# Kernel tuning notes

Hardware: AMD Instinct MI355X
Metric: run time of the kernel (lower is better)

The kernel has to match this reference:

```python
import jax, jax.numpy as jnp
import numpy as np

BLOCK_SIZE = 32
TAU = 0.1
E2M1_VALUES = np.array([0.0, 0.5, 1.0, 1.5, 2.0, 3.0, 4.0, 6.0], dtype=np.float32)
E2M1_BOUNDS = np.array([0.25, 0.75, 1.25, 1.75, 2.5, 3.5, 5.0], dtype=np.float32)


def setup_inputs() -> dict:
    key = jax.random.key(0)
    x = jax.random.normal(key, (2048, 4096), dtype=jnp.float32)
    return {
        "x": x,
        "delta_raw": jnp.zeros((), dtype=jnp.float32),
        "bounds_base": jnp.asarray(E2M1_BOUNDS),
        "values_table": jnp.asarray(E2M1_VALUES),
    }


def reference(x, delta_raw, bounds_base, values_table):
    orig_shape = x.shape
    bs = BLOCK_SIZE
    xb = x.reshape(-1, bs)  # [n_blocks, bs]
    # per-block e8m0 power-of-two scale from amax
    amax = jnp.max(jnp.abs(xb), axis=-1, keepdims=True)
    descale = amax / 6.0
    e8m0_scale = jnp.ceil(jnp.maximum(jnp.log2(descale), -127.0))
    scale_factor = jnp.exp2(e8m0_scale)
    x_scaled = (xb / scale_factor).reshape(orig_shape)
    # perturbed decision bounds
    shifted_bounds = bounds_base + 0.5 * jnp.tanh(delta_raw)  # [7]
    x_abs = jnp.abs(x_scaled)
    # hard ordinal bucketize: count bounds exceeded -> code in [0,7]
    ord_hard = jnp.sum(x_abs[..., None] > shifted_bounds, axis=-1)  # int32
    sign_bit = (x_scaled < 0).astype(jnp.uint8)
    codes = (sign_bit << 3) | ord_hard.astype(jnp.uint8)
    # soft ordinal weights via sigmoid at each boundary
    p = jax.nn.sigmoid((x_abs[..., None] - shifted_bounds) / TAU)  # [..., 7]
    w0 = 1.0 - p[..., 0]
    mids = p[..., :-1] - p[..., 1:]
    w_last = p[..., -1]
    weights = jnp.concatenate([w0[..., None], mids, w_last[..., None]], axis=-1)  # [..., 8]
    weights = jnp.clip(weights, 0.0)
    weights = weights / (jnp.sum(weights, axis=-1, keepdims=True) + 1e-8)
    abs_soft = jnp.sum(weights * values_table, axis=-1)
    abs_hard = values_table[ord_hard]
    # straight-through: hard value forward, soft gradient
    abs_mix = abs_soft + jax.lax.stop_gradient(abs_hard - abs_soft)
    y_scaled = jnp.where(x_scaled >= 0, abs_mix, -abs_mix)
    y = (y_scaled.reshape(-1, bs) * scale_factor).reshape(orig_shape)
    scales = (e8m0_scale + 127.0).astype(jnp.uint8)[:, 0].reshape(
        *orig_shape[:-1], orig_shape[-1] // bs
    )
    return (y, codes, scales, shifted_bounds, weights)
```

## Files before the change

kernel.cpp:

```cpp
#include <hip/hip_runtime.h>

#define BLK 256

__global__ __launch_bounds__(BLK) void fp4_kernel(
    const float* __restrict__ x,
    const float* __restrict__ delta_raw,
    const float* __restrict__ bounds_base,
    const float* __restrict__ values_table,
    float* __restrict__ out, long long N)
{
    const int tid = threadIdx.x;
    const long long gid = (long long)blockIdx.x * BLK + tid;

    __shared__ float s_vals[8];
    __shared__ float s_w[8 * 264];

    if (tid < 8) s_vals[tid] = values_table[tid];

    const float delta = delta_raw[0];
    const float ht = 0.5f * tanhf(delta);
    float sb[7];
#pragma unroll
    for (int j = 0; j < 7; ++j) sb[j] = bounds_base[j] + ht;

    __syncthreads();

    const float xi = x[gid];

    float a = fabsf(xi);
#pragma unroll
    for (int off = 16; off >= 1; off >>= 1)
        a = fmaxf(a, __shfl_xor(a, off, 32));

    const float descale = a / 6.0f;
    const float e = ceilf(fmaxf(log2f(descale), -127.0f));
    const float scale = exp2f(e);
    const float xs = xi / scale;
    const float xa = fabsf(xs);

    int ord = 0;
    float p[7];
#pragma unroll
    for (int j = 0; j < 7; ++j) {
        if (xa > sb[j]) ord++;
        p[j] = 1.0f / (1.0f + expf(-((xa - sb[j]) / 0.1f)));
    }

    float w[8];
    w[0] = 1.0f - p[0];
#pragma unroll
    for (int j = 1; j < 7; ++j) w[j] = p[j - 1] - p[j];
    w[7] = p[6];

    float sum = 0.0f;
#pragma unroll
    for (int k = 0; k < 8; ++k) { w[k] = fmaxf(w[k], 0.0f); sum += w[k]; }
    const float inv = 1.0f / (sum + 1e-8f);

    float abs_soft = 0.0f;
#pragma unroll
    for (int k = 0; k < 8; ++k) { w[k] *= inv; abs_soft += w[k] * s_vals[k]; }

    const float abs_hard = s_vals[ord];
    const float abs_mix = abs_soft + (abs_hard - abs_soft);
    const float ys = (xs >= 0.0f) ? abs_mix : -abs_mix;

    out[gid] = ys * scale;
    const int code = ((xs < 0.0f) ? 8 : 0) | ord;
    out[N + gid] = (float)code;
    if ((tid & 31) == 0) out[2 * N + (gid >> 5)] = e + 127.0f;
    if (blockIdx.x == 0 && tid < 7) out[2 * N + (N >> 5) + tid] = sb[tid];

#pragma unroll
    for (int j = 0; j < 8; ++j) s_w[j * 264 + tid] = w[j];
    __syncthreads();

    const long long wbase = 2 * N + (N >> 5) + 7 + (long long)blockIdx.x * (BLK * 8);
#pragma unroll
    for (int k = 0; k < 8; ++k) {
        const int g = tid + k * BLK;
        out[wbase + g] = s_w[(g & 7) * 264 + (g >> 3)];
    }
}

extern "C" void kernel_launch(void* const* d_in, const int* in_sizes, int n_in,
                              void* d_out, int out_size, void* d_ws, size_t ws_size,
                              hipStream_t stream) {
    const float* x      = (const float*)d_in[0];
    const float* delta  = (const float*)d_in[1];
    const float* bounds = (const float*)d_in[2];
    const float* vals   = (const float*)d_in[3];
    float* out = (float*)d_out;
    const long long N = (long long)in_sizes[0];
    const int nblocks = (int)(N / BLK);
    fp4_kernel<<<nblocks, BLK, 0, stream>>>(x, delta, bounds, vals, out, N);
}
```

Before: 392.1 us.

## Process four elements per thread with vector I/O and fast sigmoid intrinsics

Each thread now handles four contiguous elements loaded as a float4. The block amax reduction uses in-register max plus a 3-step shuffle over 8 lanes, where it previously took 5 shuffles. The sigmoid is rewritten as rcp(1+exp2(fma)) with a precomputed log2e/tau constant, and the divide by scale becomes a multiply by exp2(-e). The weights are written directly from registers with misaligned-offset float4/float2 stores instead of a shared-memory transpose and a second __syncthreads. This cuts instruction count and synchronization, in exchange for more registers per thread, a quarter as many blocks, and slightly different rounding from the hardware approximate exp2 and rcp.

After: 401.6 us. 1.02x slower.

```diff
diff --git a/kernel.cpp b/kernel.cpp
--- a/kernel.cpp
+++ b/kernel.cpp
@@ -1,6 +1,10 @@
 #include <hip/hip_runtime.h>
 
 #define BLK 256
+
+
+__device__ __forceinline__ float fast_rcp(float x)  { return __builtin_amdgcn_rcpf(x); }
+__device__ __forceinline__ float fast_exp2(float x) { return __builtin_amdgcn_exp2f(x); }
 
 __global__ __launch_bounds__(BLK) void fp4_kernel(
     const float* __restrict__ x,
@@ -10,77 +14,87 @@
     float* __restrict__ out, long long N)
 {
     const int tid = threadIdx.x;
-    const long long gid = (long long)blockIdx.x * BLK + tid;
+    const long long t4 = (long long)blockIdx.x * BLK + tid;
 
     __shared__ float s_vals[8];
-    __shared__ float s_w[8 * 264];
-
     if (tid < 8) s_vals[tid] = values_table[tid];
 
-    const float delta = delta_raw[0];
-    const float ht = 0.5f * tanhf(delta);
-    float sb[7];
+    const float ht = 0.5f * tanhf(delta_raw[0]);
+    const float C = 14.4269504088896340f;
+    float sb[7], sbC[7];
 #pragma unroll
-    for (int j = 0; j < 7; ++j) sb[j] = bounds_base[j] + ht;
+    for (int j = 0; j < 7; ++j) { sb[j] = bounds_base[j] + ht; sbC[j] = sb[j] * C; }
 
     __syncthreads();
 
-    const float xi = x[gid];
+    const float4 xv = reinterpret_cast<const float4*>(x)[t4];
+    float xe[4] = {xv.x, xv.y, xv.z, xv.w};
 
-    float a = fabsf(xi);
-#pragma unroll
-    for (int off = 16; off >= 1; off >>= 1)
-        a = fmaxf(a, __shfl_xor(a, off, 32));
+    float a = fmaxf(fmaxf(fabsf(xe[0]), fabsf(xe[1])), fmaxf(fabsf(xe[2]), fabsf(xe[3])));
+    a = fmaxf(a, __shfl_xor(a, 1, 8));
+    a = fmaxf(a, __shfl_xor(a, 2, 8));
+    a = fmaxf(a, __shfl_xor(a, 4, 8));
 
     const float descale = a / 6.0f;
     const float e = ceilf(fmaxf(log2f(descale), -127.0f));
     const float scale = exp2f(e);
-    const float xs = xi / scale;
-    const float xa = fabsf(xs);
+    const float inv_scale = exp2f(-e);
 
-    int ord = 0;
-    float p[7];
+    float yv[4], cv[4], wbuf[32];
+
 #pragma unroll
-    for (int j = 0; j < 7; ++j) {
-        if (xa > sb[j]) ord++;
-        p[j] = 1.0f / (1.0f + expf(-((xa - sb[j]) / 0.1f)));
+    for (int i = 0; i < 4; ++i) {
+        const float xs = xe[i] * inv_scale;
+        const float xa = fabsf(xs);
+
+        int ord = 0;
+        float p[7];
+#pragma unroll
+        for (int j = 0; j < 7; ++j) {
+            p[j] = fast_rcp(1.0f + fast_exp2(fmaf(xa, -C, sbC[j])));
+            ord += (xa > sb[j]) ? 1 : 0;
+        }
+
+        float w[8];
+        w[0] = 1.0f - p[0];
+#pragma unroll
+        for (int j = 1; j < 7; ++j) w[j] = p[j - 1] - p[j];
+        w[7] = p[6];
+
+        float sum = 0.0f;
+#pragma unroll
+        for (int k = 0; k < 8; ++k) { w[k] = fmaxf(w[k], 0.0f); sum += w[k]; }
+        const float inv = fast_rcp(sum + 1e-8f);
+
+        float abs_soft = 0.0f;
+#pragma unroll
+        for (int k = 0; k < 8; ++k) { w[k] *= inv; abs_soft += w[k] * s_vals[k]; }
+
+        const float abs_hard = s_vals[ord];
+        const float abs_mix = abs_soft + (abs_hard - abs_soft);
+        const float ys = (xs >= 0.0f) ? abs_mix : -abs_mix;
+
+        yv[i] = ys * scale;
+        cv[i] = (float)(((xs < 0.0f) ? 8 : 0) | ord);
+#pragma unroll
+        for (int k = 0; k < 8; ++k) wbuf[i * 8 + k] = w[k];
     }
 
-    float w[8];
-    w[0] = 1.0f - p[0];
-#pragma unroll
-    for (int j = 1; j < 7; ++j) w[j] = p[j - 1] - p[j];
-    w[7] = p[6];
+    reinterpret_cast<float4*>(out)[t4] = make_float4(yv[0], yv[1], yv[2], yv[3]);
+    reinterpret_cast<float4*>(out + N)[t4] = make_float4(cv[0], cv[1], cv[2], cv[3]);
 
-    float sum = 0.0f;
-#pragma unroll
-    for (int k = 0; k < 8; ++k) { w[k] = fmaxf(w[k], 0.0f); sum += w[k]; }
-    const float inv = 1.0f / (sum + 1e-8f);
-
-    float abs_soft = 0.0f;
-#pragma unroll
-    for (int k = 0; k < 8; ++k) { w[k] *= inv; abs_soft += w[k] * s_vals[k]; }
-
-    const float abs_hard = s_vals[ord];
-    const float abs_mix = abs_soft + (abs_hard - abs_soft);
-    const float ys = (xs >= 0.0f) ? abs_mix : -abs_mix;
-
-    out[gid] = ys * scale;
-    const int code = ((xs < 0.0f) ? 8 : 0) | ord;
-    out[N + gid] = (float)code;
-    if ((tid & 31) == 0) out[2 * N + (gid >> 5)] = e + 127.0f;
+    if ((tid & 7) == 0) out[2 * N + (t4 >> 3)] = e + 127.0f;
     if (blockIdx.x == 0 && tid < 7) out[2 * N + (N >> 5) + tid] = sb[tid];
 
+    const long long wb = 2 * N + (N >> 5) + 7 + 32 * t4;
+    out[wb] = wbuf[0];
+    float* wp = out + wb + 1;
 #pragma unroll
-    for (int j = 0; j < 8; ++j) s_w[j * 264 + tid] = w[j];
-    __syncthreads();
-
-    const long long wbase = 2 * N + (N >> 5) + 7 + (long long)blockIdx.x * (BLK * 8);
-#pragma unroll
-    for (int k = 0; k < 8; ++k) {
-        const int g = tid + k * BLK;
-        out[wbase + g] = s_w[(g & 7) * 264 + (g >> 3)];
-    }
+    for (int k = 0; k < 7; ++k)
+        reinterpret_cast<float4*>(wp)[k] =
+            make_float4(wbuf[4 * k + 1], wbuf[4 * k + 2], wbuf[4 * k + 3], wbuf[4 * k + 4]);
+    reinterpret_cast<float2*>(out + wb + 29)[0] = make_float2(wbuf[29], wbuf[30]);
+    out[wb + 31] = wbuf[31];
 }
 
 extern "C" void kernel_launch(void* const* d_in, const int* in_sizes, int n_in,
@@ -92,6 +106,6 @@
     const float* vals   = (const float*)d_in[3];
     float* out = (float*)d_out;
     const long long N = (long long)in_sizes[0];
-    const int nblocks = (int)(N / BLK);
+    const int nblocks = (int)(N / (4 * BLK));
     fp4_kernel<<<nblocks, BLK, 0, stream>>>(x, delta, bounds, vals, out, N);
 }
```
